# Performance work log

Measured on AMD Instinct MI355X. Metric: run time of the kernel, lower is better.

## Reference

```python
import jax, jax.numpy as jnp
import numpy as np

N, D, E = 16384, 1024, 65536
HID, H1, NCLS = 512, 8, 2


def _glorot(key, shape):
    fan = shape[0] + shape[-1]
    return jax.random.normal(key, shape, jnp.float32) * np.sqrt(2.0 / fan)


def setup_inputs() -> dict:
    key = jax.random.key(0)
    ks = jax.random.split(key, 12)
    return {
        "x": jax.random.normal(ks[0], (N, D), jnp.float32),
        "edge_index": jax.random.randint(ks[1], (2, E), 0, N, dtype=jnp.int32),
        # layer 1: GATConv((-1,-1), 512, heads=8, concat=True)
        "W1_src": _glorot(ks[2], (D, H1 * HID)),
        "W1_dst": _glorot(ks[3], (D, H1 * HID)),
        "att1_src": _glorot(ks[4], (H1, HID)),
        "att1_dst": _glorot(ks[5], (H1, HID)),
        "b1": jnp.zeros((H1 * HID,), jnp.float32),
        # layer 2: GATConv((-1,-1), 2, heads=1, concat=False)
        "W2_src": _glorot(ks[6], (H1 * HID, NCLS)),
        "W2_dst": _glorot(ks[7], (H1 * HID, NCLS)),
        "att2_src": _glorot(ks[8], (1, NCLS)),
        "att2_dst": _glorot(ks[9], (1, NCLS)),
        "b2": jnp.zeros((NCLS,), jnp.float32),
    }


def gat_layer(x, src, dst, Ws, Wd, a_s, a_d, b, heads, ch, concat):
    n = x.shape[0]
    hs = (x @ Ws).reshape(n, heads, ch)  # source-transformed feats [N,H,C]
    hd = (x @ Wd).reshape(n, heads, ch)  # dest-transformed feats  [N,H,C]
    al_s = jnp.einsum("nhc,hc->nh", hs, a_s)  # [N,H]
    al_d = jnp.einsum("nhc,hc->nh", hd, a_d)
    logits = jax.nn.leaky_relu(al_s[src] + al_d[dst], 0.2)  # [E,H]
    # segment softmax over incoming edges of each destination node
    m = jax.ops.segment_max(logits, dst, num_segments=n)
    m = jnp.where(jnp.isfinite(m), m, 0.0)
    e = jnp.exp(logits - m[dst])
    denom = jax.ops.segment_sum(e, dst, num_segments=n)
    alpha = e / (denom[dst] + 1e-16)  # [E,H]
    msg = hs[src] * alpha[:, :, None]  # [E,H,C]
    out = jax.ops.segment_sum(msg, dst, num_segments=n)  # [N,H,C]
    out = out.reshape(n, heads * ch) if concat else out.mean(axis=1)
    return out + b


def reference(x, edge_index, W1_src, W1_dst, att1_src, att1_dst, b1,
              W2_src, W2_dst, att2_src, att2_dst, b2):
    n = x.shape[0]
    # PyG GATConv adds self-loops by default
    loops = jnp.arange(n, dtype=edge_index.dtype)
    src = jnp.concatenate([edge_index[0], loops])
    dst = jnp.concatenate([edge_index[1], loops])
    h = gat_layer(x, src, dst, W1_src, W1_dst, att1_src, att1_dst, b1,
                  H1, HID, concat=True)  # [N, 4096]
    out = gat_layer(h, src, dst, W2_src, W2_dst, att2_src, att2_dst, b2,
                    1, NCLS, concat=False)  # [N, 2]
    return out
```

## Files before the change

kernel.cpp:

```cpp
#include <hip/hip_runtime.h>
#include <cstdint>
#include <cstddef>

#define DEV __device__ __forceinline__

typedef __attribute__((ext_vector_type(8))) short bf16x8;
typedef __attribute__((ext_vector_type(4))) float f32x4;

constexpr int N_  = 16384;
constexpr int D_  = 1024;
constexpr int E_  = 65536;
constexpr int ET_ = E_ + N_;
constexpr int H_  = 8;
constexpr int C_  = 512;
constexpr int F_  = 4096;
constexpr int ZS_ = 48;
constexpr int KSPLIT = 2;

DEV unsigned short f2bf(float f){
  unsigned u = __float_as_uint(f);
  unsigned r = u + 0x7FFFu + ((u >> 16) & 1u);
  return (unsigned short)(r >> 16);
}
DEV float lrelu(float x){ return x >= 0.f ? x : 0.2f * x; }
DEV float waveSum(float v){
  #pragma unroll
  for (int o = 32; o > 0; o >>= 1) v += __shfl_xor(v, o);
  return v;
}
DEV int eSRC(const int* ei, int e){ return e < E_ ? ei[e]      : e - E_; }
DEV int eDST(const int* ei, int e){ return e < E_ ? ei[E_ + e] : e - E_; }

__global__ void init_all(uint4* __restrict__ zr, int n16,
                         const float* __restrict__ W2d, const float* __restrict__ a2d,
                         float* __restrict__ wd2){
  int i = blockIdx.x * blockDim.x + threadIdx.x;
  if (i < n16){ uint4 z = {0u,0u,0u,0u}; zr[i] = z; }
  if (i < F_) wd2[i] = W2d[i * 2] * a2d[0] + W2d[i * 2 + 1] * a2d[1];
}

__global__ __launch_bounds__(256) void build_Vcb(
    const float* __restrict__ W1s, const float* __restrict__ W1d,
    const float* __restrict__ a1s, const float* __restrict__ a1d,
    const float* __restrict__ W2s, const float* __restrict__ wd2,
    const float* __restrict__ b1,
    unsigned short* __restrict__ Vb, float* __restrict__ cb){
  int t = threadIdx.x;
  if (blockIdx.x == D_ * H_ / 4){
    __shared__ float red[3][4];
    int w = t >> 6, lane = t & 63;
    float p0 = 0.f, p1 = 0.f, pd = 0.f;
    for (int k = t; k < F_; k += 256){
      float b = b1[k];
      p0 += b * W2s[k * 2]; p1 += b * W2s[k * 2 + 1]; pd += b * wd2[k];
    }
    p0 = waveSum(p0); p1 = waveSum(p1); pd = waveSum(pd);
    if (lane == 0){ red[0][w] = p0; red[1][w] = p1; red[2][w] = pd; }
    __syncthreads();
    if (t == 0){
      cb[0] = red[0][0] + red[0][1] + red[0][2] + red[0][3];
      cb[1] = red[1][0] + red[1][1] + red[1][2] + red[1][3];
      cb[2] = red[2][0] + red[2][1] + red[2][2] + red[2][3];
    }
    return;
  }
  int id = blockIdx.x * 4 + (t >> 6);
  int lane = t & 63;
  int d = id >> 3, h = id & 7;
  float sa = 0.f, sb = 0.f, s0 = 0.f, s1 = 0.f, sd = 0.f;
  #pragma unroll
  for (int i = 0; i < C_ / 64; i++){
    int c = i * 64 + lane;
    int gc = h * C_ + c;
    float ws  = W1s[(size_t)d * F_ + gc];
    float wdv = W1d[(size_t)d * F_ + gc];
    sa += ws * a1s[gc]; sb += wdv * a1d[gc];
    float2 w2 = *reinterpret_cast<const float2*>(W2s + (size_t)gc * 2);
    s0 += ws * w2.x; s1 += ws * w2.y; sd += ws * wd2[gc];
  }
  sa = waveSum(sa); sb = waveSum(sb);
  s0 = waveSum(s0); s1 = waveSum(s1); sd = waveSum(sd);
  if (lane == 0){
    int kc = d >> 5, ks = (d >> 3) & 3, ii = d & 7;
    auto put = [&](int jj, float v){
      int tt = jj >> 4, j = jj & 15;
      Vb[((size_t)(tt * 32 + kc) * 64 + ks * 16 + j) * 8 + ii] = f2bf(v);
    };
    put(h, sa); put(8 + h, sb); put(16 + h, s0); put(24 + h, s1); put(32 + h, sd);
  }
}

__global__ __launch_bounds__(64) void node_mfma(const float* __restrict__ X,
                                                const unsigned short* __restrict__ Vb,
                                                float* __restrict__ Z){
  int lane = threadIdx.x;
  int n0 = blockIdx.x * 16;
  int kh = blockIdx.y;
  int row = lane & 15, ks = lane >> 4;
  f32x4 ac0 = {0.f,0.f,0.f,0.f}, ac1 = ac0, ac2 = ac0;
  const float* xp = X + (size_t)(n0 + row) * D_ + ks * 8;
  constexpr int KC = 32 / KSPLIT;
  #pragma unroll 2
  for (int kk = 0; kk < KC; kk++){
    int kc = kh * KC + kk;
    float4 xa = *reinterpret_cast<const float4*>(xp + kc * 32);
    float4 xb = *reinterpret_cast<const float4*>(xp + kc * 32 + 4);
    bf16x8 a;
    a[0] = (short)f2bf(xa.x); a[1] = (short)f2bf(xa.y);
    a[2] = (short)f2bf(xa.z); a[3] = (short)f2bf(xa.w);
    a[4] = (short)f2bf(xb.x); a[5] = (short)f2bf(xb.y);
    a[6] = (short)f2bf(xb.z); a[7] = (short)f2bf(xb.w);
    bf16x8 b0 = *reinterpret_cast<const bf16x8*>(&Vb[((size_t)( 0 + kc) * 64 + lane) * 8]);
    bf16x8 b1 = *reinterpret_cast<const bf16x8*>(&Vb[((size_t)(32 + kc) * 64 + lane) * 8]);
    bf16x8 b2 = *reinterpret_cast<const bf16x8*>(&Vb[((size_t)(64 + kc) * 64 + lane) * 8]);
    ac0 = __builtin_amdgcn_mfma_f32_16x16x32_bf16(a, b0, ac0, 0, 0, 0);
    ac1 = __builtin_amdgcn_mfma_f32_16x16x32_bf16(a, b1, ac1, 0, 0, 0);
    ac2 = __builtin_amdgcn_mfma_f32_16x16x32_bf16(a, b2, ac2, 0, 0, 0);
  }
  #pragma unroll
  for (int r = 0; r < 4; r++){
    int n = n0 + ks * 4 + r;
    atomicAdd(&Z[(size_t)n * ZS_ +  0 + row], ac0[r]);
    atomicAdd(&Z[(size_t)n * ZS_ + 16 + row], ac1[r]);
    atomicAdd(&Z[(size_t)n * ZS_ + 32 + row], ac2[r]);
  }
}

__global__ void edge1(const int* __restrict__ ei, const float* __restrict__ Z,
                      float* __restrict__ den1, float* __restrict__ a0,
                      float* __restrict__ a1, float* __restrict__ ad){
  int t = blockIdx.x * blockDim.x + threadIdx.x;
  if (t >= ET_ * H_) return;
  int e = t >> 3, h = t & 7;
  int s = eSRC(ei, e), d = eDST(ei, e);
  const float* zs = Z + (size_t)s * ZS_;
  float ev = expf(lrelu(zs[h] + Z[(size_t)d * ZS_ + 8 + h]));
  int o = d * 8 + h;
  atomicAdd(&den1[o], ev);
  atomicAdd(&a0[o], ev * zs[16 + h]);
  atomicAdd(&a1[o], ev * zs[24 + h]);
  atomicAdd(&ad[o], ev * zs[32 + h]);
}

__global__ void node_mid(const float* __restrict__ den1, const float* __restrict__ a0,
                         const float* __restrict__ a1, const float* __restrict__ ad,
                         const float* __restrict__ cb, const float* __restrict__ a2s,
                         float4* __restrict__ Pn){
  int n = blockIdx.x * blockDim.x + threadIdx.x;
  if (n >= N_) return;
  float v0 = 0.f, v1 = 0.f, vd = 0.f;
  #pragma unroll
  for (int h = 0; h < 8; h++){
    float inv = 1.f / (den1[n * 8 + h] + 1e-16f);
    v0 += a0[n * 8 + h] * inv;
    v1 += a1[n * 8 + h] * inv;
    vd += ad[n * 8 + h] * inv;
  }
  v0 += cb[0]; v1 += cb[1]; vd += cb[2];
  float4 r;
  r.x = v0 * a2s[0] + v1 * a2s[1];
  r.y = v0; r.z = v1;
  r.w = vd;
  Pn[n] = r;
}

__global__ void edge2(const int* __restrict__ ei, const float4* __restrict__ Pn,
                      float* __restrict__ den2, float* __restrict__ o0,
                      float* __restrict__ o1){
  int e = blockIdx.x * blockDim.x + threadIdx.x;
  if (e >= ET_) return;
  int s = eSRC(ei, e), d = eDST(ei, e);
  float4 ps = Pn[s];
  float ald = Pn[d].w;
  float ev = expf(lrelu(ps.x + ald));
  atomicAdd(&den2[d], ev);
  atomicAdd(&o0[d], ev * ps.y);
  atomicAdd(&o1[d], ev * ps.z);
}

__global__ void node_out(const float* __restrict__ den2, const float* __restrict__ o0,
                         const float* __restrict__ o1, const float* __restrict__ b2,
                         float* __restrict__ out){
  int n = blockIdx.x * blockDim.x + threadIdx.x;
  if (n >= N_) return;
  float inv = 1.f / (den2[n] + 1e-16f);
  out[2 * n]     = o0[n] * inv + b2[0];
  out[2 * n + 1] = o1[n] * inv + b2[1];
}

extern "C" void kernel_launch(void* const* d_in, const int* in_sizes, int n_in,
                              void* d_out, int out_size, void* d_ws, size_t ws_size,
                              hipStream_t stream){
  const float* x   = (const float*)d_in[0];
  const int*   ei  = (const int*)  d_in[1];
  const float* W1s = (const float*)d_in[2];
  const float* W1d = (const float*)d_in[3];
  const float* a1s = (const float*)d_in[4];
  const float* a1d = (const float*)d_in[5];
  const float* b1  = (const float*)d_in[6];
  const float* W2s = (const float*)d_in[7];
  const float* W2d = (const float*)d_in[8];
  const float* a2s = (const float*)d_in[9];
  const float* a2d = (const float*)d_in[10];
  const float* b2  = (const float*)d_in[11];
  float* out = (float*)d_out;

  char* p = (char*)d_ws;
  auto alloc = [&](size_t bytes) -> void* {
    void* r = (void*)p;
    p += (bytes + 255) & ~(size_t)255;
    return r;
  };
  float* Z     = (float*)alloc((size_t)N_ * ZS_ * 4);
  float* den1  = (float*)alloc((size_t)N_ * H_ * 4);
  float* a0    = (float*)alloc((size_t)N_ * H_ * 4);
  float* a1    = (float*)alloc((size_t)N_ * H_ * 4);
  float* ad    = (float*)alloc((size_t)N_ * H_ * 4);
  float* den2  = (float*)alloc((size_t)N_ * 4);
  float* o0    = (float*)alloc((size_t)N_ * 4);
  float* o1    = (float*)alloc((size_t)N_ * 4);
  unsigned short* Vb = (unsigned short*)alloc((size_t)3 * 32 * 64 * 8 * 2);
  float* wd2   = (float*)alloc((size_t)F_ * 4);
  float* cb    = (float*)alloc(256);
  float4* Pn   = (float4*)alloc((size_t)N_ * 16);

  size_t zrBytes = (size_t)((char*)wd2 - (char*)Z);
  int n16 = (int)(zrBytes / 16);
  int g1 = (int)((((n16 > F_) ? n16 : F_) + 255) / 256);

  init_all<<<dim3(g1), dim3(256), 0, stream>>>((uint4*)Z, n16, W2d, a2d, wd2);
  build_Vcb<<<dim3(D_ * H_ / 4 + 1), dim3(256), 0, stream>>>(W1s, W1d, a1s, a1d,
                                                             W2s, wd2, b1, Vb, cb);
  node_mfma<<<dim3(N_ / 16, KSPLIT), dim3(64), 0, stream>>>(x, Vb, Z);
  edge1<<<dim3(ET_ * H_ / 256), dim3(256), 0, stream>>>(ei, Z, den1, a0, a1, ad);
  node_mid<<<dim3(N_ / 256), dim3(256), 0, stream>>>(den1, a0, a1, ad, cb, a2s, Pn);
  edge2<<<dim3(ET_ / 256), dim3(256), 0, stream>>>(ei, Pn, den2, o0, o1);
  node_out<<<dim3(N_ / 256), dim3(256), 0, stream>>>(den2, o0, o1, b2, out);
}
```

Before: 73.89 us.

## Fuse init into prep kernel, fold node_mid into edge2, raise K-split

```diff
diff --git a/kernel.cpp b/kernel.cpp
--- a/kernel.cpp
+++ b/kernel.cpp
@@ -15,7 +15,8 @@
 constexpr int C_  = 512;
 constexpr int F_  = 4096;
 constexpr int ZS_ = 48;
-constexpr int KSPLIT = 2;
+constexpr int KSPLIT = 4;
+constexpr int NVB = 2048;
 
 DEV unsigned short f2bf(float f){
   unsigned u = __float_as_uint(f);
@@ -31,28 +32,53 @@
 DEV int eSRC(const int* ei, int e){ return e < E_ ? ei[e]      : e - E_; }
 DEV int eDST(const int* ei, int e){ return e < E_ ? ei[E_ + e] : e - E_; }
 
-__global__ void init_all(uint4* __restrict__ zr, int n16,
-                         const float* __restrict__ W2d, const float* __restrict__ a2d,
-                         float* __restrict__ wd2){
-  int i = blockIdx.x * blockDim.x + threadIdx.x;
-  if (i < n16){ uint4 z = {0u,0u,0u,0u}; zr[i] = z; }
-  if (i < F_) wd2[i] = W2d[i * 2] * a2d[0] + W2d[i * 2 + 1] * a2d[1];
-}
-
-__global__ __launch_bounds__(256) void build_Vcb(
+__global__ __launch_bounds__(256) void prep(
     const float* __restrict__ W1s, const float* __restrict__ W1d,
     const float* __restrict__ a1s, const float* __restrict__ a1d,
-    const float* __restrict__ W2s, const float* __restrict__ wd2,
-    const float* __restrict__ b1,
-    unsigned short* __restrict__ Vb, float* __restrict__ cb){
+    const float* __restrict__ W2s, const float* __restrict__ W2d,
+    const float* __restrict__ a2d, const float* __restrict__ b1,
+    unsigned short* __restrict__ Vb, float* __restrict__ cb,
+    uint4* __restrict__ zr, int n16){
   int t = threadIdx.x;
-  if (blockIdx.x == D_ * H_ / 4){
+  int bx = blockIdx.x;
+  if (bx < NVB){
+    int id = bx * 4 + (t >> 6);
+    int lane = t & 63;
+    int d = id >> 3, h = id & 7;
+    float a2d0 = a2d[0], a2d1 = a2d[1];
+    float sa = 0.f, sb = 0.f, s0 = 0.f, s1 = 0.f, sd = 0.f;
+    #pragma unroll
+    for (int i = 0; i < C_ / 64; i++){
+      int c = i * 64 + lane;
+      int gc = h * C_ + c;
+      float ws  = W1s[(size_t)d * F_ + gc];
+      float wdv = W1d[(size_t)d * F_ + gc];
+      sa += ws * a1s[gc]; sb += wdv * a1d[gc];
+      float2 w2 = *reinterpret_cast<const float2*>(W2s + (size_t)gc * 2);
+      float2 wx = *reinterpret_cast<const float2*>(W2d + (size_t)gc * 2);
+      s0 += ws * w2.x; s1 += ws * w2.y;
+      sd += ws * (wx.x * a2d0 + wx.y * a2d1);
+    }
+    sa = waveSum(sa); sb = waveSum(sb);
+    s0 = waveSum(s0); s1 = waveSum(s1); sd = waveSum(sd);
+    if (lane == 0){
+      int kc = d >> 5, ks = (d >> 3) & 3, ii = d & 7;
+      auto put = [&](int jj, float v){
+        int tt = jj >> 4, j = jj & 15;
+        Vb[((size_t)(tt * 32 + kc) * 64 + ks * 16 + j) * 8 + ii] = f2bf(v);
+      };
+      put(h, sa); put(8 + h, sb); put(16 + h, s0); put(24 + h, s1); put(32 + h, sd);
+    }
+  } else if (bx == NVB){
     __shared__ float red[3][4];
     int w = t >> 6, lane = t & 63;
+    float a2d0 = a2d[0], a2d1 = a2d[1];
     float p0 = 0.f, p1 = 0.f, pd = 0.f;
     for (int k = t; k < F_; k += 256){
       float b = b1[k];
-      p0 += b * W2s[k * 2]; p1 += b * W2s[k * 2 + 1]; pd += b * wd2[k];
+      float2 w2 = *reinterpret_cast<const float2*>(W2s + (size_t)k * 2);
+      float2 wx = *reinterpret_cast<const float2*>(W2d + (size_t)k * 2);
+      p0 += b * w2.x; p1 += b * w2.y; pd += b * (wx.x * a2d0 + wx.y * a2d1);
     }
     p0 = waveSum(p0); p1 = waveSum(p1); pd = waveSum(pd);
     if (lane == 0){ red[0][w] = p0; red[1][w] = p1; red[2][w] = pd; }
@@ -62,31 +88,9 @@
       cb[1] = red[1][0] + red[1][1] + red[1][2] + red[1][3];
       cb[2] = red[2][0] + red[2][1] + red[2][2] + red[2][3];
     }
-    return;
-  }
-  int id = blockIdx.x * 4 + (t >> 6);
-  int lane = t & 63;
-  int d = id >> 3, h = id & 7;
-  float sa = 0.f, sb = 0.f, s0 = 0.f, s1 = 0.f, sd = 0.f;
-  #pragma unroll
-  for (int i = 0; i < C_ / 64; i++){
-    int c = i * 64 + lane;
-    int gc = h * C_ + c;
-    float ws  = W1s[(size_t)d * F_ + gc];
-    float wdv = W1d[(size_t)d * F_ + gc];
-    sa += ws * a1s[gc]; sb += wdv * a1d[gc];
-    float2 w2 = *reinterpret_cast<const float2*>(W2s + (size_t)gc * 2);
-    s0 += ws * w2.x; s1 += ws * w2.y; sd += ws * wd2[gc];
-  }
-  sa = waveSum(sa); sb = waveSum(sb);
-  s0 = waveSum(s0); s1 = waveSum(s1); sd = waveSum(sd);
-  if (lane == 0){
-    int kc = d >> 5, ks = (d >> 3) & 3, ii = d & 7;
-    auto put = [&](int jj, float v){
-      int tt = jj >> 4, j = jj & 15;
-      Vb[((size_t)(tt * 32 + kc) * 64 + ks * 16 + j) * 8 + ii] = f2bf(v);
-    };
-    put(h, sa); put(8 + h, sb); put(16 + h, s0); put(24 + h, s1); put(32 + h, sd);
+  } else {
+    int i = (bx - NVB - 1) * 256 + t;
+    if (i < n16){ uint4 z = {0u, 0u, 0u, 0u}; zr[i] = z; }
   }
 }
 
@@ -142,40 +146,42 @@
   atomicAdd(&ad[o], ev * zs[32 + h]);
 }
 
-__global__ void node_mid(const float* __restrict__ den1, const float* __restrict__ a0,
-                         const float* __restrict__ a1, const float* __restrict__ ad,
-                         const float* __restrict__ cb, const float* __restrict__ a2s,
-                         float4* __restrict__ Pn){
-  int n = blockIdx.x * blockDim.x + threadIdx.x;
-  if (n >= N_) return;
-  float v0 = 0.f, v1 = 0.f, vd = 0.f;
-  #pragma unroll
-  for (int h = 0; h < 8; h++){
-    float inv = 1.f / (den1[n * 8 + h] + 1e-16f);
-    v0 += a0[n * 8 + h] * inv;
-    v1 += a1[n * 8 + h] * inv;
-    vd += ad[n * 8 + h] * inv;
-  }
-  v0 += cb[0]; v1 += cb[1]; vd += cb[2];
-  float4 r;
-  r.x = v0 * a2s[0] + v1 * a2s[1];
-  r.y = v0; r.z = v1;
-  r.w = vd;
-  Pn[n] = r;
-}
-
-__global__ void edge2(const int* __restrict__ ei, const float4* __restrict__ Pn,
+__global__ void edge2(const int* __restrict__ ei, const float* __restrict__ den1,
+                      const float* __restrict__ a0, const float* __restrict__ a1,
+                      const float* __restrict__ ad, const float* __restrict__ cb,
+                      const float* __restrict__ a2s,
                       float* __restrict__ den2, float* __restrict__ o0,
                       float* __restrict__ o1){
   int e = blockIdx.x * blockDim.x + threadIdx.x;
   if (e >= ET_) return;
   int s = eSRC(ei, e), d = eDST(ei, e);
-  float4 ps = Pn[s];
-  float ald = Pn[d].w;
-  float ev = expf(lrelu(ps.x + ald));
+  float4 dsa = *reinterpret_cast<const float4*>(den1 + (size_t)s * 8);
+  float4 dsb = *reinterpret_cast<const float4*>(den1 + (size_t)s * 8 + 4);
+  float4 a0a = *reinterpret_cast<const float4*>(a0 + (size_t)s * 8);
+  float4 a0b = *reinterpret_cast<const float4*>(a0 + (size_t)s * 8 + 4);
+  float4 a1a = *reinterpret_cast<const float4*>(a1 + (size_t)s * 8);
+  float4 a1b = *reinterpret_cast<const float4*>(a1 + (size_t)s * 8 + 4);
+  float i0 = 1.f/(dsa.x+1e-16f), i1 = 1.f/(dsa.y+1e-16f);
+  float i2 = 1.f/(dsa.z+1e-16f), i3 = 1.f/(dsa.w+1e-16f);
+  float i4 = 1.f/(dsb.x+1e-16f), i5 = 1.f/(dsb.y+1e-16f);
+  float i6 = 1.f/(dsb.z+1e-16f), i7 = 1.f/(dsb.w+1e-16f);
+  float v0 = cb[0] + a0a.x*i0 + a0a.y*i1 + a0a.z*i2 + a0a.w*i3
+                   + a0b.x*i4 + a0b.y*i5 + a0b.z*i6 + a0b.w*i7;
+  float v1 = cb[1] + a1a.x*i0 + a1a.y*i1 + a1a.z*i2 + a1a.w*i3
+                   + a1b.x*i4 + a1b.y*i5 + a1b.z*i6 + a1b.w*i7;
+  float4 dda = *reinterpret_cast<const float4*>(den1 + (size_t)d * 8);
+  float4 ddb = *reinterpret_cast<const float4*>(den1 + (size_t)d * 8 + 4);
+  float4 ada = *reinterpret_cast<const float4*>(ad + (size_t)d * 8);
+  float4 adb = *reinterpret_cast<const float4*>(ad + (size_t)d * 8 + 4);
+  float vd = cb[2] + ada.x/(dda.x+1e-16f) + ada.y/(dda.y+1e-16f)
+                   + ada.z/(dda.z+1e-16f) + ada.w/(dda.w+1e-16f)
+                   + adb.x/(ddb.x+1e-16f) + adb.y/(ddb.y+1e-16f)
+                   + adb.z/(ddb.z+1e-16f) + adb.w/(ddb.w+1e-16f);
+  float als = v0 * a2s[0] + v1 * a2s[1];
+  float ev = expf(lrelu(als + vd));
   atomicAdd(&den2[d], ev);
-  atomicAdd(&o0[d], ev * ps.y);
-  atomicAdd(&o1[d], ev * ps.z);
+  atomicAdd(&o0[d], ev * v0);
+  atomicAdd(&o1[d], ev * v1);
 }
 
 __global__ void node_out(const float* __restrict__ den2, const float* __restrict__ o0,
@@ -220,20 +226,17 @@
   float* o0    = (float*)alloc((size_t)N_ * 4);
   float* o1    = (float*)alloc((size_t)N_ * 4);
   unsigned short* Vb = (unsigned short*)alloc((size_t)3 * 32 * 64 * 8 * 2);
-  float* wd2   = (float*)alloc((size_t)F_ * 4);
   float* cb    = (float*)alloc(256);
-  float4* Pn   = (float4*)alloc((size_t)N_ * 16);
-
-  size_t zrBytes = (size_t)((char*)wd2 - (char*)Z);
+
+  size_t zrBytes = (size_t)((char*)Vb - (char*)Z);
   int n16 = (int)(zrBytes / 16);
-  int g1 = (int)((((n16 > F_) ? n16 : F_) + 255) / 256);
-
-  init_all<<<dim3(g1), dim3(256), 0, stream>>>((uint4*)Z, n16, W2d, a2d, wd2);
-  build_Vcb<<<dim3(D_ * H_ / 4 + 1), dim3(256), 0, stream>>>(W1s, W1d, a1s, a1d,
-                                                             W2s, wd2, b1, Vb, cb);
+  int nzb = (n16 + 255) / 256;
+
+  prep<<<dim3(NVB + 1 + nzb), dim3(256), 0, stream>>>(W1s, W1d, a1s, a1d, W2s, W2d,
+                                                      a2d, b1, Vb, cb, (uint4*)Z, n16);
   node_mfma<<<dim3(N_ / 16, KSPLIT), dim3(64), 0, stream>>>(x, Vb, Z);
   edge1<<<dim3(ET_ * H_ / 256), dim3(256), 0, stream>>>(ei, Z, den1, a0, a1, ad);
-  node_mid<<<dim3(N_ / 256), dim3(256), 0, stream>>>(den1, a0, a1, ad, cb, a2s, Pn);
-  edge2<<<dim3(ET_ / 256), dim3(256), 0, stream>>>(ei, Pn, den2, o0, o1);
+  edge2<<<dim3(ET_ / 256), dim3(256), 0, stream>>>(ei, den1, a0, a1, ad, cb, a2s,
+                                                   den2, o0, o1);
   node_out<<<dim3(N_ / 256), dim3(256), 0, stream>>>(den2, o0, o1, b2, out);
 }
```

After: 71.45 us. 1.03x faster.
